# Optimization experiments

Measured on AMD Instinct MI355X. Metric: run time of the kernel, lower is better.

Reference implementation:

```python
import jax, jax.numpy as jnp
import numpy as np

RADIUS = 4
SIGMA1 = 5.0
SIGMA2 = 1.0


def _gauss_1d(radius, sigma):
    x = jnp.arange(-radius, radius + 1, dtype=jnp.float32)
    return jnp.exp(-(x ** 2) / (2.0 * sigma ** 2))  # peak-1 gaussian (norm.pdf(d)/norm.pdf(0))


def _blur3d(x, g, radius):
    # Separable 3D gaussian conv; product of 1D kernels == exp(-(dx^2+dy^2+dz^2)/(2*sigma^2)),
    # mathematically identical to the dense (2r+1)^3 conv3d in the torch module.
    dn = ('NCDHW', 'OIDHW', 'NCDHW')
    for ax in range(3):
        shape = [1, 1, 1, 1, 1]
        shape[2 + ax] = g.shape[0]
        k = g.reshape(shape)
        pad = [(0, 0), (0, 0), (0, 0)]
        pad[ax] = (radius, radius)
        x = jax.lax.conv_general_dilated(x, k, (1, 1, 1), pad, dimension_numbers=dn)
    return x


def setup_inputs() -> dict:
    key = jax.random.key(0)
    k1, k2 = jax.random.split(key)
    labels = jax.random.uniform(k1, (2, 4, 128, 128, 128), dtype=jnp.float32)
    inputs = jax.random.normal(k2, (2, 1, 128, 128, 128), dtype=jnp.float32)
    return {"labels": labels, "inputs": inputs}


def reference(labels, inputs):
    num_classes = labels.shape[1]
    g = _gauss_1d(RADIUS, SIGMA1)
    loss = jnp.float32(0.0)
    for k in range(num_classes):
        class_probs = labels[:, k:k + 1]  # [B,1,D,H,W]
        class_mean = (jnp.mean(inputs * class_probs, axis=(2, 3, 4), keepdims=True)
                      / (jnp.mean(class_probs, axis=(2, 3, 4), keepdims=True) + 1e-5))  # [B,C,1,1,1]
        diff = jnp.sum((inputs - class_mean) ** 2, axis=1, keepdims=True)  # [B,1,D,H,W]
        weights = jnp.exp(-(diff ** 2) / (SIGMA2 ** 2))
        numerator = jnp.sum(class_probs * _blur3d(class_probs * weights, g, RADIUS))
        denominator = jnp.sum(class_probs * _blur3d(weights, g, RADIUS))
        # L1Loss(x, 0) on a scalar == |x|
        loss = loss + jnp.abs(numerator / (denominator + 1e-6))
    return num_classes - loss
```

## Files before the change

kernel.cpp:

```cpp
#include <hip/hip_runtime.h>
#include <math.h>

#define DIM   128
#define SLICE (DIM*DIM)
#define VOL   (DIM*DIM*DIM)
#define NK    4
#define NVOL  8
#define SSTR  33

__constant__ float c_g[9] = {
    0.72614904f, 0.83527021f, 0.92311635f, 0.98019867f, 1.0f,
    0.98019867f, 0.92311635f, 0.83527021f, 0.72614904f
};


__global__ __launch_bounds__(256) void k_sums(
    const float* __restrict__ labels, const float* __restrict__ inputs,
    float* __restrict__ red)
{
    const int b     = blockIdx.x >> 9;
    const int chunk = blockIdx.x & 511;
    const int t     = threadIdx.x;
    const size_t off4 = (size_t)chunk*1024 + t;
    const float4* __restrict__ I4 = (const float4*)inputs + (size_t)b*(VOL/4) + off4;
    const float4* __restrict__ L4 = (const float4*)labels;
    float sp[4] = {0,0,0,0}, sip[4] = {0,0,0,0};
    #pragma unroll
    for (int j = 0; j < 4; ++j) {
        const float4 iv = I4[j*256];
        #pragma unroll
        for (int k = 0; k < 4; ++k) {
            const float4 p = L4[(size_t)(b*NK + k)*(VOL/4) + off4 + j*256];
            sp[k]  += p.x + p.y + p.z + p.w;
            sip[k] += p.x*iv.x + p.y*iv.y + p.z*iv.z + p.w*iv.w;
        }
    }
    #pragma unroll
    for (int k = 0; k < 4; ++k) {
        #pragma unroll
        for (int o = 32; o; o >>= 1) {
            sp[k]  += __shfl_down(sp[k],  o);
            sip[k] += __shfl_down(sip[k], o);
        }
    }
    __shared__ float sB[8][4];
    const int wid = t >> 6;
    if ((t & 63) == 0) {
        #pragma unroll
        for (int k = 0; k < 4; ++k) { sB[k][wid] = sp[k]; sB[4+k][wid] = sip[k]; }
    }
    __syncthreads();
    if (t < 8) {
        const float v = sB[t][0] + sB[t][1] + sB[t][2] + sB[t][3];
        atomicAdd(&red[(t < 4 ? 0 : 8) + b*NK + (t & 3)], v);
    }
}

__global__ __launch_bounds__(256) void k_fused(
    const float* __restrict__ labels, const float* __restrict__ inputs,
    const float* __restrict__ red, float* __restrict__ nd)
{
    __shared__ float4 sW[2][16*SSTR + 8];
    __shared__ float sN[4], sD[4];

    const int dq    = blockIdx.x & 3;
    const int strip = (blockIdx.x >> 2) & 15;
    const int vol   = blockIdx.x >> 6;
    const int b = vol >> 2, kcls = vol & 3;
    const int d0 = dq * 32;
    const int t  = threadIdx.x;
    const float g1 = c_g[5], g2 = c_g[6], g3 = c_g[7], g4 = c_g[8];
    const float4 z4 = make_float4(0.f, 0.f, 0.f, 0.f);

    const float* __restrict__ src = labels + (size_t)vol*VOL;
    const float mean = red[8+vol] / (red[vol] + 20.97152f);

    const int r0 = t >> 5, c0 = t & 31;
    const int r1 = r0 + 8;
    const int ho = t >> 5, wq = t & 31;

    const int hA = strip*8 - 4 + r0;
    const int hB = strip*8 - 4 + r1;
    const bool vA = (unsigned)hA < 128u;
    const bool vB = (unsigned)hB < 128u;
    const float4* __restrict__ rowA = (const float4*)(src + (size_t)(vA ? hA : 0)*DIM);
    const float4* __restrict__ rowB = (const float4*)(src + (size_t)(vB ? hB : 0)*DIM);

    const size_t ob4 = (size_t)(strip*8 + ho)*(DIM/4) + wq;
    const float4* __restrict__ P4 = (const float4*)src + ob4;
    const float4* __restrict__ I4 = (const float4*)(inputs + (size_t)b*VOL) + ob4;

    float4 ring[9];
    #pragma unroll
    for (int i = 0; i < 9; ++i) ring[i] = z4;
    float numAcc = 0.f, denAcc = 0.f;

    auto ldA = [&](int s, float4& pv, float4& cv, float4& nx) {
        pv = cv = nx = z4;
        if (vA && (unsigned)s < 128u) {
            const float4* rp = rowA + (size_t)s*(SLICE/4);
            cv = rp[c0];
            if (c0 > 0)  pv = rp[c0-1];
            if (c0 < 31) nx = rp[c0+1];
        }
    };
    auto ldB = [&](int s, float4& pv, float4& cv, float4& nx) {
        pv = cv = nx = z4;
        if (vB && (unsigned)s < 128u) {
            const float4* rp = rowB + (size_t)s*(SLICE/4);
            cv = rp[c0];
            if (c0 > 0)  pv = rp[c0-1];
            if (c0 < 31) nx = rp[c0+1];
        }
    };

    float4 Apv, Acv, Anx, Bpv, Bcv, Bnx;
    ldA(d0-4, Apv, Acv, Anx);
    ldB(d0-4, Bpv, Bcv, Bnx);

    #pragma unroll 2
    for (int s = d0-4; s < d0+36; ++s) {
        const float4 apv=Apv, acv=Acv, anx=Anx, bpv=Bpv, bcv=Bcv, bnx=Bnx;
        ldA(s+1, Apv, Acv, Anx);
        ldB(s+1, Bpv, Bcv, Bnx);
        float4 pc = z4, ic = z4;
        const bool outStep = (s >= d0+4);
        if (outStep) {
            pc = P4[(size_t)(s-4)*(SLICE/4)];
            ic = I4[(size_t)(s-4)*(SLICE/4)];
        }
        const int buf = s & 1;
        {
            float4 o;
            o.x = acv.x + g1*(apv.w+acv.y) + g2*(apv.z+acv.z) + g3*(apv.y+acv.w) + g4*(apv.x+anx.x);
            o.y = acv.y + g1*(acv.x+acv.z) + g2*(apv.w+acv.w) + g3*(apv.z+anx.x) + g4*(apv.y+anx.y);
            o.z = acv.z + g1*(acv.y+acv.w) + g2*(acv.x+anx.x) + g3*(apv.w+anx.y) + g4*(apv.z+anx.z);
            o.w = acv.w + g1*(acv.z+anx.x) + g2*(acv.y+anx.y) + g3*(acv.x+anx.z) + g4*(apv.w+anx.w);
            sW[buf][r0*SSTR + c0] = o;
        }
        {
            float4 o;
            o.x = bcv.x + g1*(bpv.w+bcv.y) + g2*(bpv.z+bcv.z) + g3*(bpv.y+bcv.w) + g4*(bpv.x+bnx.x);
            o.y = bcv.y + g1*(bcv.x+bcv.z) + g2*(bpv.w+bcv.w) + g3*(bpv.z+bnx.x) + g4*(bpv.y+bnx.y);
            o.z = bcv.z + g1*(bcv.y+bcv.w) + g2*(bcv.x+bnx.x) + g3*(bpv.w+bnx.y) + g4*(bpv.z+bnx.z);
            o.w = bcv.w + g1*(bcv.z+bnx.x) + g2*(bcv.y+bnx.y) + g3*(bcv.x+bnx.z) + g4*(bpv.w+bnx.w);
            sW[buf][r1*SSTR + c0] = o;
        }
        __syncthreads();
        float4 acc = sW[buf][(ho+4)*SSTR + wq];
        #pragma unroll
        for (int dt = 1; dt <= 4; ++dt) {
            const float g = c_g[4+dt];
            const float4 u = sW[buf][(ho+4-dt)*SSTR + wq];
            const float4 v = sW[buf][(ho+4+dt)*SSTR + wq];
            acc.x += g*(u.x+v.x); acc.y += g*(u.y+v.y);
            acc.z += g*(u.z+v.z); acc.w += g*(u.w+v.w);
        }
        #pragma unroll
        for (int i = 0; i < 8; ++i) ring[i] = ring[i+1];
        ring[8] = acc;
        if (outStep) {
            float4 B = ring[4];
            #pragma unroll
            for (int dt = 1; dt <= 4; ++dt) {
                const float g = c_g[4+dt];
                B.x += g*(ring[4+dt].x + ring[4-dt].x);
                B.y += g*(ring[4+dt].y + ring[4-dt].y);
                B.z += g*(ring[4+dt].z + ring[4-dt].z);
                B.w += g*(ring[4+dt].w + ring[4-dt].w);
            }
            { float df = ic.x - mean; df *= df; const float bw = B.x * __expf(-df*df); numAcc += bw*pc.x; denAcc += bw; }
            { float df = ic.y - mean; df *= df; const float bw = B.y * __expf(-df*df); numAcc += bw*pc.y; denAcc += bw; }
            { float df = ic.z - mean; df *= df; const float bw = B.z * __expf(-df*df); numAcc += bw*pc.z; denAcc += bw; }
            { float df = ic.w - mean; df *= df; const float bw = B.w * __expf(-df*df); numAcc += bw*pc.w; denAcc += bw; }
        }
    }

    #pragma unroll
    for (int o = 32; o; o >>= 1) { numAcc += __shfl_down(numAcc, o); denAcc += __shfl_down(denAcc, o); }
    if ((t & 63) == 0) { sN[t >> 6] = numAcc; sD[t >> 6] = denAcc; }
    __syncthreads();
    if (t == 0) {
        atomicAdd(&nd[kcls],   sN[0]+sN[1]+sN[2]+sN[3]);
        atomicAdd(&nd[4+kcls], sD[0]+sD[1]+sD[2]+sD[3]);
    }
}

__global__ void k_final(const float* __restrict__ red, float* __restrict__ out)
{
    float loss = 0.f;
    #pragma unroll
    for (int k = 0; k < 4; ++k) loss += fabsf(red[16+k] / (red[20+k] + 1e-6f));
    out[0] = (float)NK - loss;
}

extern "C" void kernel_launch(void* const* d_in, const int* in_sizes, int n_in,
                              void* d_out, int out_size, void* d_ws, size_t ws_size,
                              hipStream_t stream)
{
    const float* labels = (const float*)d_in[0];
    const float* inputs = (const float*)d_in[1];
    float* out = (float*)d_out;
    float* red = (float*)d_ws;

    hipMemsetAsync(red, 0, 24*sizeof(float), stream);
    k_sums<<<2*512, 256, 0, stream>>>(labels, inputs, red);
    k_fused<<<NVOL*16*4, 256, 0, stream>>>(labels, inputs, red, red + 16);
    k_final<<<1, 1, 0, stream>>>(red, out);
}
```

Measured before the change: 183.5 us.

## Process two depth slices per barrier, pad atomics, fold final kernel into last block

The fused blur loop now handles two depth slices per iteration. It uses a doubled shared-memory buffer and a 10-entry register ring, which halves the number of __syncthreads calls and raises memory-level parallelism. Reduction counters are spaced 32 floats apart to avoid atomic contention on shared cache lines. The separate final kernel is removed: a last-block-done counter with a threadfence lets the final block compute the loss. The changes also add launch_bounds(256,2), and the larger register footprint and shared memory could reduce occupancy.

Result: no change. 185.4 us (+1.0%).

```diff
diff --git a/kernel.cpp b/kernel.cpp
--- a/kernel.cpp
+++ b/kernel.cpp
@@ -5,8 +5,9 @@
 #define SLICE (DIM*DIM)
 #define VOL   (DIM*DIM*DIM)
 #define NK    4
-#define NVOL  8
 #define SSTR  33
+#define WSS   32
+#define DONE  24
 
 __constant__ float c_g[9] = {
     0.72614904f, 0.83527021f, 0.92311635f, 0.98019867f, 1.0f,
@@ -52,15 +53,15 @@
     __syncthreads();
     if (t < 8) {
         const float v = sB[t][0] + sB[t][1] + sB[t][2] + sB[t][3];
-        atomicAdd(&red[(t < 4 ? 0 : 8) + b*NK + (t & 3)], v);
+        atomicAdd(&red[((t < 4 ? 0 : 8) + b*NK + (t & 3))*WSS], v);
     }
 }
 
-__global__ __launch_bounds__(256) void k_fused(
+__global__ __launch_bounds__(256, 2) void k_fused(
     const float* __restrict__ labels, const float* __restrict__ inputs,
-    const float* __restrict__ red, float* __restrict__ nd)
+    float* __restrict__ red, float* __restrict__ out)
 {
-    __shared__ float4 sW[2][16*SSTR + 8];
+    __shared__ float4 sW[2][2][16*SSTR + 8];
     __shared__ float sN[4], sD[4];
 
     const int dq    = blockIdx.x & 3;
@@ -73,7 +74,7 @@
     const float4 z4 = make_float4(0.f, 0.f, 0.f, 0.f);
 
     const float* __restrict__ src = labels + (size_t)vol*VOL;
-    const float mean = red[8+vol] / (red[vol] + 20.97152f);
+    const float mean = red[(8+vol)*WSS] / (red[vol*WSS] + 20.97152f);
 
     const int r0 = t >> 5, c0 = t & 31;
     const int r1 = r0 + 8;
@@ -90,9 +91,9 @@
     const float4* __restrict__ P4 = (const float4*)src + ob4;
     const float4* __restrict__ I4 = (const float4*)(inputs + (size_t)b*VOL) + ob4;
 
-    float4 ring[9];
-    #pragma unroll
-    for (int i = 0; i < 9; ++i) ring[i] = z4;
+    float4 ring[10];
+    #pragma unroll
+    for (int i = 0; i < 10; ++i) ring[i] = z4;
     float numAcc = 0.f, denAcc = 0.f;
 
     auto ldA = [&](int s, float4& pv, float4& cv, float4& nx) {
@@ -114,65 +115,85 @@
         }
     };
 
-    float4 Apv, Acv, Anx, Bpv, Bcv, Bnx;
-    ldA(d0-4, Apv, Acv, Anx);
-    ldB(d0-4, Bpv, Bcv, Bnx);
-
-    #pragma unroll 2
-    for (int s = d0-4; s < d0+36; ++s) {
-        const float4 apv=Apv, acv=Acv, anx=Anx, bpv=Bpv, bcv=Bcv, bnx=Bnx;
-        ldA(s+1, Apv, Acv, Anx);
-        ldB(s+1, Bpv, Bcv, Bnx);
-        float4 pc = z4, ic = z4;
-        const bool outStep = (s >= d0+4);
+    auto wblur = [&](const float4& pv, const float4& cv, const float4& nx) {
+        float4 o;
+        o.x = cv.x + g1*(pv.w+cv.y) + g2*(pv.z+cv.z) + g3*(pv.y+cv.w) + g4*(pv.x+nx.x);
+        o.y = cv.y + g1*(cv.x+cv.z) + g2*(pv.w+cv.w) + g3*(pv.z+nx.x) + g4*(pv.y+nx.y);
+        o.z = cv.z + g1*(cv.y+cv.w) + g2*(cv.x+nx.x) + g3*(pv.w+nx.y) + g4*(pv.z+nx.z);
+        o.w = cv.w + g1*(cv.z+nx.x) + g2*(cv.y+nx.y) + g3*(cv.x+nx.z) + g4*(pv.w+nx.w);
+        return o;
+    };
+
+    float4 A0pv,A0cv,A0nx, B0pv,B0cv,B0nx;
+    float4 A1pv,A1cv,A1nx, B1pv,B1cv,B1nx;
+    ldA(d0-4, A0pv,A0cv,A0nx);  ldB(d0-4, B0pv,B0cv,B0nx);
+    ldA(d0-3, A1pv,A1cv,A1nx);  ldB(d0-3, B1pv,B1cv,B1nx);
+
+    int pp = 0;
+    for (int s0 = d0-4; s0 < d0+36; s0 += 2, pp ^= 1) {
+        sW[pp][0][r0*SSTR + c0] = wblur(A0pv,A0cv,A0nx);
+        sW[pp][0][r1*SSTR + c0] = wblur(B0pv,B0cv,B0nx);
+        ldA(s0+2, A0pv,A0cv,A0nx);
+        ldB(s0+2, B0pv,B0cv,B0nx);
+        sW[pp][1][r0*SSTR + c0] = wblur(A1pv,A1cv,A1nx);
+        sW[pp][1][r1*SSTR + c0] = wblur(B1pv,B1cv,B1nx);
+        ldA(s0+3, A1pv,A1cv,A1nx);
+        ldB(s0+3, B1pv,B1cv,B1nx);
+
+        const bool outStep = (s0 >= d0+4);
+        float4 pc0 = z4, ic0 = z4, pc1 = z4, ic1 = z4;
         if (outStep) {
-            pc = P4[(size_t)(s-4)*(SLICE/4)];
-            ic = I4[(size_t)(s-4)*(SLICE/4)];
-        }
-        const int buf = s & 1;
-        {
-            float4 o;
-            o.x = acv.x + g1*(apv.w+acv.y) + g2*(apv.z+acv.z) + g3*(apv.y+acv.w) + g4*(apv.x+anx.x);
-            o.y = acv.y + g1*(acv.x+acv.z) + g2*(apv.w+acv.w) + g3*(apv.z+anx.x) + g4*(apv.y+anx.y);
-            o.z = acv.z + g1*(acv.y+acv.w) + g2*(acv.x+anx.x) + g3*(apv.w+anx.y) + g4*(apv.z+anx.z);
-            o.w = acv.w + g1*(acv.z+anx.x) + g2*(acv.y+anx.y) + g3*(acv.x+anx.z) + g4*(apv.w+anx.w);
-            sW[buf][r0*SSTR + c0] = o;
-        }
-        {
-            float4 o;
-            o.x = bcv.x + g1*(bpv.w+bcv.y) + g2*(bpv.z+bcv.z) + g3*(bpv.y+bcv.w) + g4*(bpv.x+bnx.x);
-            o.y = bcv.y + g1*(bcv.x+bcv.z) + g2*(bpv.w+bcv.w) + g3*(bpv.z+bnx.x) + g4*(bpv.y+bnx.y);
-            o.z = bcv.z + g1*(bcv.y+bcv.w) + g2*(bcv.x+bnx.x) + g3*(bpv.w+bnx.y) + g4*(bpv.z+bnx.z);
-            o.w = bcv.w + g1*(bcv.z+bnx.x) + g2*(bcv.y+bnx.y) + g3*(bcv.x+bnx.z) + g4*(bpv.w+bnx.w);
-            sW[buf][r1*SSTR + c0] = o;
-        }
+            pc0 = P4[(size_t)(s0-4)*(SLICE/4)];
+            ic0 = I4[(size_t)(s0-4)*(SLICE/4)];
+            pc1 = P4[(size_t)(s0-3)*(SLICE/4)];
+            ic1 = I4[(size_t)(s0-3)*(SLICE/4)];
+        }
+
         __syncthreads();
-        float4 acc = sW[buf][(ho+4)*SSTR + wq];
+
+        float4 acc0 = sW[pp][0][(ho+4)*SSTR + wq];
+        float4 acc1 = sW[pp][1][(ho+4)*SSTR + wq];
         #pragma unroll
         for (int dt = 1; dt <= 4; ++dt) {
             const float g = c_g[4+dt];
-            const float4 u = sW[buf][(ho+4-dt)*SSTR + wq];
-            const float4 v = sW[buf][(ho+4+dt)*SSTR + wq];
-            acc.x += g*(u.x+v.x); acc.y += g*(u.y+v.y);
-            acc.z += g*(u.z+v.z); acc.w += g*(u.w+v.w);
-        }
-        #pragma unroll
-        for (int i = 0; i < 8; ++i) ring[i] = ring[i+1];
-        ring[8] = acc;
+            const float4 u0 = sW[pp][0][(ho+4-dt)*SSTR + wq];
+            const float4 v0 = sW[pp][0][(ho+4+dt)*SSTR + wq];
+            acc0.x += g*(u0.x+v0.x); acc0.y += g*(u0.y+v0.y);
+            acc0.z += g*(u0.z+v0.z); acc0.w += g*(u0.w+v0.w);
+            const float4 u1 = sW[pp][1][(ho+4-dt)*SSTR + wq];
+            const float4 v1 = sW[pp][1][(ho+4+dt)*SSTR + wq];
+            acc1.x += g*(u1.x+v1.x); acc1.y += g*(u1.y+v1.y);
+            acc1.z += g*(u1.z+v1.z); acc1.w += g*(u1.w+v1.w);
+        }
+
+        #pragma unroll
+        for (int i = 0; i < 8; ++i) ring[i] = ring[i+2];
+        ring[8] = acc0;
+        ring[9] = acc1;
+
         if (outStep) {
-            float4 B = ring[4];
+            float4 B0 = ring[4];
+            float4 B1 = ring[5];
             #pragma unroll
             for (int dt = 1; dt <= 4; ++dt) {
                 const float g = c_g[4+dt];
-                B.x += g*(ring[4+dt].x + ring[4-dt].x);
-                B.y += g*(ring[4+dt].y + ring[4-dt].y);
-                B.z += g*(ring[4+dt].z + ring[4-dt].z);
-                B.w += g*(ring[4+dt].w + ring[4-dt].w);
+                B0.x += g*(ring[4+dt].x + ring[4-dt].x);
+                B0.y += g*(ring[4+dt].y + ring[4-dt].y);
+                B0.z += g*(ring[4+dt].z + ring[4-dt].z);
+                B0.w += g*(ring[4+dt].w + ring[4-dt].w);
+                B1.x += g*(ring[5+dt].x + ring[5-dt].x);
+                B1.y += g*(ring[5+dt].y + ring[5-dt].y);
+                B1.z += g*(ring[5+dt].z + ring[5-dt].z);
+                B1.w += g*(ring[5+dt].w + ring[5-dt].w);
             }
-            { float df = ic.x - mean; df *= df; const float bw = B.x * __expf(-df*df); numAcc += bw*pc.x; denAcc += bw; }
-            { float df = ic.y - mean; df *= df; const float bw = B.y * __expf(-df*df); numAcc += bw*pc.y; denAcc += bw; }
-            { float df = ic.z - mean; df *= df; const float bw = B.z * __expf(-df*df); numAcc += bw*pc.z; denAcc += bw; }
-            { float df = ic.w - mean; df *= df; const float bw = B.w * __expf(-df*df); numAcc += bw*pc.w; denAcc += bw; }
+            { float df = ic0.x - mean; df *= df; const float bw = B0.x * __expf(-df*df); numAcc += bw*pc0.x; denAcc += bw; }
+            { float df = ic0.y - mean; df *= df; const float bw = B0.y * __expf(-df*df); numAcc += bw*pc0.y; denAcc += bw; }
+            { float df = ic0.z - mean; df *= df; const float bw = B0.z * __expf(-df*df); numAcc += bw*pc0.z; denAcc += bw; }
+            { float df = ic0.w - mean; df *= df; const float bw = B0.w * __expf(-df*df); numAcc += bw*pc0.w; denAcc += bw; }
+            { float df = ic1.x - mean; df *= df; const float bw = B1.x * __expf(-df*df); numAcc += bw*pc1.x; denAcc += bw; }
+            { float df = ic1.y - mean; df *= df; const float bw = B1.y * __expf(-df*df); numAcc += bw*pc1.y; denAcc += bw; }
+            { float df = ic1.z - mean; df *= df; const float bw = B1.z * __expf(-df*df); numAcc += bw*pc1.z; denAcc += bw; }
+            { float df = ic1.w - mean; df *= df; const float bw = B1.w * __expf(-df*df); numAcc += bw*pc1.w; denAcc += bw; }
         }
     }
 
@@ -181,17 +202,21 @@
     if ((t & 63) == 0) { sN[t >> 6] = numAcc; sD[t >> 6] = denAcc; }
     __syncthreads();
     if (t == 0) {
-        atomicAdd(&nd[kcls],   sN[0]+sN[1]+sN[2]+sN[3]);
-        atomicAdd(&nd[4+kcls], sD[0]+sD[1]+sD[2]+sD[3]);
-    }
-}
-
-__global__ void k_final(const float* __restrict__ red, float* __restrict__ out)
-{
-    float loss = 0.f;
-    #pragma unroll
-    for (int k = 0; k < 4; ++k) loss += fabsf(red[16+k] / (red[20+k] + 1e-6f));
-    out[0] = (float)NK - loss;
+        atomicAdd(&red[(16+kcls)*WSS], sN[0]+sN[1]+sN[2]+sN[3]);
+        atomicAdd(&red[(20+kcls)*WSS], sD[0]+sD[1]+sD[2]+sD[3]);
+        __threadfence();
+        const unsigned old = atomicAdd((unsigned int*)&red[DONE*WSS], 1u);
+        if (old == 511u) {
+            float loss = 0.f;
+            #pragma unroll
+            for (int k = 0; k < 4; ++k) {
+                const float nu = atomicAdd(&red[(16+k)*WSS], 0.0f);
+                const float de = atomicAdd(&red[(20+k)*WSS], 0.0f);
+                loss += fabsf(nu / (de + 1e-6f));
+            }
+            out[0] = (float)NK - loss;
+        }
+    }
 }
 
 extern "C" void kernel_launch(void* const* d_in, const int* in_sizes, int n_in,
@@ -203,8 +228,7 @@
     float* out = (float*)d_out;
     float* red = (float*)d_ws;
 
-    hipMemsetAsync(red, 0, 24*sizeof(float), stream);
+    hipMemsetAsync(red, 0, 25*WSS*sizeof(float), stream);
     k_sums<<<2*512, 256, 0, stream>>>(labels, inputs, red);
-    k_fused<<<NVOL*16*4, 256, 0, stream>>>(labels, inputs, red, red + 16);
-    k_final<<<1, 1, 0, stream>>>(red, out);
+    k_fused<<<8*16*4, 256, 0, stream>>>(labels, inputs, red, out);
 }
```

## Software-pipeline LDS stages, fold final reduction into last block, pad atomics

Applied to the files above, without the earlier changes.

Each H-blur stage now writes one shared buffer while the vertical pass reads the other, written in the previous iteration. The loop runs one extra step and needs only a single barrier per iteration instead of the barrier between write and read. The separate k_final launch is replaced by a completion counter, so the last block computes the loss. Atomic accumulators are padded to separate cache lines, and launch bounds request two blocks per CU. This adds a counter, a fence and one extra pipeline step per block.

Measured after the change: 708.4 us. 286% more time.

```diff
diff --git a/kernel.cpp b/kernel.cpp
--- a/kernel.cpp
+++ b/kernel.cpp
@@ -5,8 +5,9 @@
 #define SLICE (DIM*DIM)
 #define VOL   (DIM*DIM*DIM)
 #define NK    4
-#define NVOL  8
 #define SSTR  33
+#define WSS   32
+#define DONE  24
 
 __constant__ float c_g[9] = {
     0.72614904f, 0.83527021f, 0.92311635f, 0.98019867f, 1.0f,
@@ -52,13 +53,13 @@
     __syncthreads();
     if (t < 8) {
         const float v = sB[t][0] + sB[t][1] + sB[t][2] + sB[t][3];
-        atomicAdd(&red[(t < 4 ? 0 : 8) + b*NK + (t & 3)], v);
+        atomicAdd(&red[((t < 4 ? 0 : 8) + b*NK + (t & 3))*WSS], v);
     }
 }
 
-__global__ __launch_bounds__(256) void k_fused(
+__global__ __launch_bounds__(256, 2) void k_fused(
     const float* __restrict__ labels, const float* __restrict__ inputs,
-    const float* __restrict__ red, float* __restrict__ nd)
+    float* __restrict__ red, float* __restrict__ out)
 {
     __shared__ float4 sW[2][16*SSTR + 8];
     __shared__ float sN[4], sD[4];
@@ -73,7 +74,7 @@
     const float4 z4 = make_float4(0.f, 0.f, 0.f, 0.f);
 
     const float* __restrict__ src = labels + (size_t)vol*VOL;
-    const float mean = red[8+vol] / (red[vol] + 20.97152f);
+    const float mean = red[(8+vol)*WSS] / (red[vol*WSS] + 20.97152f);
 
     const int r0 = t >> 5, c0 = t & 31;
     const int r1 = r0 + 8;
@@ -119,24 +120,24 @@
     ldB(d0-4, Bpv, Bcv, Bnx);
 
     #pragma unroll 2
-    for (int s = d0-4; s < d0+36; ++s) {
+    for (int s = d0-4; s <= d0+36; ++s) {
         const float4 apv=Apv, acv=Acv, anx=Anx, bpv=Bpv, bcv=Bcv, bnx=Bnx;
         ldA(s+1, Apv, Acv, Anx);
         ldB(s+1, Bpv, Bcv, Bnx);
         float4 pc = z4, ic = z4;
-        const bool outStep = (s >= d0+4);
+        const bool outStep = (s >= d0+5);
         if (outStep) {
-            pc = P4[(size_t)(s-4)*(SLICE/4)];
-            ic = I4[(size_t)(s-4)*(SLICE/4)];
-        }
-        const int buf = s & 1;
+            pc = P4[(size_t)(s-5)*(SLICE/4)];
+            ic = I4[(size_t)(s-5)*(SLICE/4)];
+        }
+        const int bw = s & 1, br = bw ^ 1;
         {
             float4 o;
             o.x = acv.x + g1*(apv.w+acv.y) + g2*(apv.z+acv.z) + g3*(apv.y+acv.w) + g4*(apv.x+anx.x);
             o.y = acv.y + g1*(acv.x+acv.z) + g2*(apv.w+acv.w) + g3*(apv.z+anx.x) + g4*(apv.y+anx.y);
             o.z = acv.z + g1*(acv.y+acv.w) + g2*(acv.x+anx.x) + g3*(apv.w+anx.y) + g4*(apv.z+anx.z);
             o.w = acv.w + g1*(acv.z+anx.x) + g2*(acv.y+anx.y) + g3*(acv.x+anx.z) + g4*(apv.w+anx.w);
-            sW[buf][r0*SSTR + c0] = o;
+            sW[bw][r0*SSTR + c0] = o;
         }
         {
             float4 o;
@@ -144,15 +145,14 @@
             o.y = bcv.y + g1*(bcv.x+bcv.z) + g2*(bpv.w+bcv.w) + g3*(bpv.z+bnx.x) + g4*(bpv.y+bnx.y);
             o.z = bcv.z + g1*(bcv.y+bcv.w) + g2*(bcv.x+bnx.x) + g3*(bpv.w+bnx.y) + g4*(bpv.z+bnx.z);
             o.w = bcv.w + g1*(bcv.z+bnx.x) + g2*(bcv.y+bnx.y) + g3*(bcv.x+bnx.z) + g4*(bpv.w+bnx.w);
-            sW[buf][r1*SSTR + c0] = o;
-        }
-        __syncthreads();
-        float4 acc = sW[buf][(ho+4)*SSTR + wq];
+            sW[bw][r1*SSTR + c0] = o;
+        }
+        float4 acc = sW[br][(ho+4)*SSTR + wq];
         #pragma unroll
         for (int dt = 1; dt <= 4; ++dt) {
             const float g = c_g[4+dt];
-            const float4 u = sW[buf][(ho+4-dt)*SSTR + wq];
-            const float4 v = sW[buf][(ho+4+dt)*SSTR + wq];
+            const float4 u = sW[br][(ho+4-dt)*SSTR + wq];
+            const float4 v = sW[br][(ho+4+dt)*SSTR + wq];
             acc.x += g*(u.x+v.x); acc.y += g*(u.y+v.y);
             acc.z += g*(u.z+v.z); acc.w += g*(u.w+v.w);
         }
@@ -169,11 +169,12 @@
                 B.z += g*(ring[4+dt].z + ring[4-dt].z);
                 B.w += g*(ring[4+dt].w + ring[4-dt].w);
             }
-            { float df = ic.x - mean; df *= df; const float bw = B.x * __expf(-df*df); numAcc += bw*pc.x; denAcc += bw; }
-            { float df = ic.y - mean; df *= df; const float bw = B.y * __expf(-df*df); numAcc += bw*pc.y; denAcc += bw; }
-            { float df = ic.z - mean; df *= df; const float bw = B.z * __expf(-df*df); numAcc += bw*pc.z; denAcc += bw; }
-            { float df = ic.w - mean; df *= df; const float bw = B.w * __expf(-df*df); numAcc += bw*pc.w; denAcc += bw; }
-        }
+            { float df = ic.x - mean; df *= df; const float bwt = B.x * __expf(-df*df); numAcc += bwt*pc.x; denAcc += bwt; }
+            { float df = ic.y - mean; df *= df; const float bwt = B.y * __expf(-df*df); numAcc += bwt*pc.y; denAcc += bwt; }
+            { float df = ic.z - mean; df *= df; const float bwt = B.z * __expf(-df*df); numAcc += bwt*pc.z; denAcc += bwt; }
+            { float df = ic.w - mean; df *= df; const float bwt = B.w * __expf(-df*df); numAcc += bwt*pc.w; denAcc += bwt; }
+        }
+        __syncthreads();
     }
 
     #pragma unroll
@@ -181,17 +182,21 @@
     if ((t & 63) == 0) { sN[t >> 6] = numAcc; sD[t >> 6] = denAcc; }
     __syncthreads();
     if (t == 0) {
-        atomicAdd(&nd[kcls],   sN[0]+sN[1]+sN[2]+sN[3]);
-        atomicAdd(&nd[4+kcls], sD[0]+sD[1]+sD[2]+sD[3]);
-    }
-}
-
-__global__ void k_final(const float* __restrict__ red, float* __restrict__ out)
-{
-    float loss = 0.f;
-    #pragma unroll
-    for (int k = 0; k < 4; ++k) loss += fabsf(red[16+k] / (red[20+k] + 1e-6f));
-    out[0] = (float)NK - loss;
+        atomicAdd(&red[(16+kcls)*WSS], sN[0]+sN[1]+sN[2]+sN[3]);
+        atomicAdd(&red[(20+kcls)*WSS], sD[0]+sD[1]+sD[2]+sD[3]);
+        __threadfence();
+        const unsigned old = atomicAdd((unsigned int*)&red[DONE*WSS], 1u);
+        if (old == 511u) {
+            float loss = 0.f;
+            #pragma unroll
+            for (int k = 0; k < 4; ++k) {
+                const float nu = atomicAdd(&red[(16+k)*WSS], 0.0f);
+                const float de = atomicAdd(&red[(20+k)*WSS], 0.0f);
+                loss += fabsf(nu / (de + 1e-6f));
+            }
+            out[0] = (float)NK - loss;
+        }
+    }
 }
 
 extern "C" void kernel_launch(void* const* d_in, const int* in_sizes, int n_in,
@@ -203,8 +208,7 @@
     float* out = (float*)d_out;
     float* red = (float*)d_ws;
 
-    hipMemsetAsync(red, 0, 24*sizeof(float), stream);
+    hipMemsetAsync(red, 0, 25*WSS*sizeof(float), stream);
     k_sums<<<2*512, 256, 0, stream>>>(labels, inputs, red);
-    k_fused<<<NVOL*16*4, 256, 0, stream>>>(labels, inputs, red, red + 16);
-    k_final<<<1, 1, 0, stream>>>(red, out);
+    k_fused<<<8*16*4, 256, 0, stream>>>(labels, inputs, red, out);
 }
```
